# Kernel tuning notes

Measured on AMD Instinct MI355X. Metric: run time of the kernel, lower is better.

The kernel has to match this reference:

```python
import jax, jax.numpy as jnp
import numpy as np
from jax import lax

R = 25          # top-k hard attention cutoff
LBP_DAMP = 0.5  # damping factor for loopy BP
LBP_ITER = 5    # number of message-passing rounds
M, C, W, D = 400, 8, 100, 300  # mentions, candidates, ctxt window, vec size
H = 100         # nn_pem_interm_size


def setup_inputs() -> dict:
    key = jax.random.key(0)
    ks = jax.random.split(key, 12)
    ctxt_words = jax.random.randint(ks[0], (M, W), 0, 300000)
    ctxt_words_vec = jax.random.normal(ks[1], (M, W, D), jnp.float32)
    cand_entities = jax.random.randint(ks[2], (M, C), 0, 300000)
    cand_entities_vec = jax.random.normal(ks[3], (M, C, D), jnp.float32)
    p_e_m = -jax.random.uniform(ks[4], (M, C), jnp.float32) * 5.0  # log p(e|m)
    # learned params (A/B/C init to ones in torch; perturb slightly for generality)
    A_linear = 1.0 + 0.02 * jax.random.normal(ks[5], (D,), jnp.float32)
    B_linear = 1.0 + 0.02 * jax.random.normal(ks[6], (D,), jnp.float32)
    C_linear = 1.0 + 0.02 * jax.random.normal(ks[7], (D,), jnp.float32)
    W1 = jax.random.normal(ks[8], (H, 2), jnp.float32) * 0.5
    b1 = jax.random.normal(ks[9], (H,), jnp.float32) * 0.1
    W2 = jax.random.normal(ks[10], (1, H), jnp.float32) * 0.1
    b2 = jax.random.normal(ks[11], (1,), jnp.float32) * 0.1
    return {
        "ctxt_words": ctxt_words, "ctxt_words_vec": ctxt_words_vec,
        "cand_entities": cand_entities, "cand_entities_vec": cand_entities_vec,
        "p_e_m": p_e_m,
        "A_linear": A_linear, "B_linear": B_linear, "C_linear": C_linear,
        "W1": W1, "b1": b1, "W2": W2, "b2": b2,
    }


def _entity_context(ctxt_words_vec, cand_entities_vec, A_linear, B_linear):
    # u_vec[m,c,w] = <A*e_mc, w_mw>
    pre_u = cand_entities_vec * A_linear                       # [M,C,D]
    u_vec = jnp.einsum('mcd,mwd->mcw', pre_u, ctxt_words_vec)  # [M,C,W]
    u = u_vec.max(axis=1)                                      # [M,W]
    top_k = lax.top_k(u, R)[0]                                 # [M,R] sorted desc
    sketch = top_k[:, R - 1][:, None]                          # R-th largest
    minus = u - sketch
    minus = jnp.where(minus > 0, minus, -50.0)  # Threshold(0, -50)
    minus = minus + sketch
    beta = jax.nn.softmax(minus, axis=1)                        # [M,W]
    ctxt_full = jnp.einsum('mwd,mw->md', ctxt_words_vec, beta)  # [M,D]
    scores = jnp.einsum('mcd,md->mc', cand_entities_vec, ctxt_full * B_linear)
    return scores, beta


def reference(ctxt_words, ctxt_words_vec, cand_entities, cand_entities_vec,
              p_e_m, A_linear, B_linear, C_linear, W1, b1, W2, b2):
    scores, beta = _entity_context(ctxt_words_vec, cand_entities_vec,
                                   A_linear, B_linear)          # [M,C]
    # pairwise entity-entity scores
    flat = cand_entities_vec.reshape(M * C, D)
    pairwise = ((flat * C_linear) @ flat.T).reshape(M, C, M, C)  # [M,C,M,C]
    # unary[a,b,m,c] = scores[m,c]
    up = pairwise + scores[None, None, :, :]                     # [M,C,M,C]

    msg = jnp.zeros((M, C, M), jnp.float32)
    # mask[j,:,j] = 0 (self-exclusion)
    mask = 1.0 - jnp.eye(M, dtype=jnp.float32)[:, None, :]       # [M,1,M]
    for _ in range(LBP_ITER):
        crf_old = (1.0 - LBP_DAMP) * jnp.exp(msg)                # [M,C,M]
        s = msg.sum(axis=2)                                      # [M,C]
        new = up + s[None, None, :, :]                           # [M,C,M,C]
        sel = new.max(axis=3)                                    # [M,C,M]
        sel = jax.nn.log_softmax(sel, axis=1)
        sel = sel * mask
        msg = jnp.log(jnp.exp(sel) * LBP_DAMP + crf_old)

    global_message = msg.sum(axis=2)                             # [M,C]
    fgs = jax.nn.log_softmax(scores + global_message, axis=-1)   # [M,C]
    x = jnp.stack([fgs.reshape(-1), p_e_m.reshape(-1)], axis=1)  # [M*C,2]
    x = jax.nn.relu(x @ W1.T + b1)                               # [M*C,H]
    x = x @ W2.T + b2                                            # [M*C,1]
    return x.reshape(M, C)
```

## Files before the change

kernel.cpp:

```cpp
#include <hip/hip_runtime.h>
#include <hip/hip_bf16.h>
#include <math.h>

#define Mm 400
#define Cc 8
#define Ww 100
#define Dd 300
#define Hh 100
#define Rr 25
#define MC 3200
#define KP 320
#define LBP_ITERS 5
#define CTX_STRIDE 688

typedef _Float16 f16x8 __attribute__((ext_vector_type(8)));
typedef _Float16 f16x4 __attribute__((ext_vector_type(4)));
typedef float f32x4 __attribute__((ext_vector_type(4)));

__device__ __forceinline__ void gload16(const void* g, void* l) {
  __builtin_amdgcn_global_load_lds(
      (const __attribute__((address_space(1))) void*)g,
      (__attribute__((address_space(3))) void*)l, 16, 0, 0);
}

__global__ __launch_bounds__(256) void k_convert(
    const float* __restrict__ X,
    const float* __restrict__ Cl,
    const float* __restrict__ A,
    _Float16* __restrict__ Ah,
    _Float16* __restrict__ Bh,
    _Float16* __restrict__ AhA)
{
  int idx = blockIdx.x * 256 + threadIdx.x;
  if (idx >= MC * KP) return;
  int j = idx / KP, k = idx - j * KP;
  float x = 0.f, cl = 0.f, a = 0.f;
  if (k < Dd) { x = X[(size_t)j * Dd + k]; cl = Cl[k]; a = A[k]; }
  Bh[idx]  = (_Float16)x;
  Ah[idx]  = (_Float16)(x * cl);
  AhA[idx] = (_Float16)(x * a);
}

__global__ __launch_bounds__(64) void k_u(
    const float* __restrict__ ctxt_vec,
    const _Float16* __restrict__ candA,
    float* __restrict__ u)
{
  const int bx = blockIdx.x, m = blockIdx.y;
  const int w0 = bx * 16;
  const int tid = threadIdx.x;
  const int fr = tid & 15, fq = tid >> 4;
  __shared__ __align__(16) _Float16 candH[16 * (CTX_STRIDE / 2)];
  __shared__ __align__(16) _Float16 ctxtH[16 * (CTX_STRIDE / 2)];

  const _Float16* ca = candA + (size_t)m * Cc * KP;
#pragma unroll
  for (int e = tid; e < 320; e += 64) {
    int r = e / 40, j = e - r * 40;
    f16x8 v = *(const f16x8*)(ca + r * KP + j * 8);
    *(f16x8*)((char*)candH + r * CTX_STRIDE + j * 16) = v;
  }
  const float* cw = ctxt_vec + (size_t)m * Ww * Dd;
  const int nr = (w0 + 16 <= Ww) ? 16 : (Ww - w0);
  for (int e = tid; e < nr * 75; e += 64) {
    int r = e / 75, j = e - r * 75;
    float4 v = *(const float4*)(cw + (size_t)(w0 + r) * Dd + j * 4);
    f16x4 h = { (_Float16)v.x, (_Float16)v.y, (_Float16)v.z, (_Float16)v.w };
    *(f16x4*)((char*)ctxtH + r * CTX_STRIDE + j * 8) = h;
  }
  for (int e = tid; e < nr * 5; e += 64) {
    int r = e / 5, q = e - r * 5;
    f16x4 z = {};
    *(f16x4*)((char*)ctxtH + r * CTX_STRIDE + 600 + q * 8) = z;
  }
  __syncthreads();

  f32x4 acc = {};
#pragma unroll
  for (int s = 0; s < 10; ++s) {
    int kb = s * 64 + fq * 16;
    f16x8 af = *(const f16x8*)((const char*)candH + fr * CTX_STRIDE + kb);
    f16x8 bf = *(const f16x8*)((const char*)ctxtH + fr * CTX_STRIDE + kb);
    acc = __builtin_amdgcn_mfma_f32_16x16x32_f16(af, bf, acc, 0, 0, 0);
  }
  float v0 = fmaxf(fmaxf(acc[0], acc[1]), fmaxf(acc[2], acc[3]));
  if (fq >= 2) v0 = -1e30f;
  v0 = fmaxf(v0, __shfl_xor(v0, 16));
  if (fq == 0 && (w0 + fr) < Ww) u[m * 128 + w0 + fr] = v0;
}

__global__ __launch_bounds__(512) void k_escore(
    const float* __restrict__ u,
    const float* __restrict__ ctxt_vec,
    const float* __restrict__ cand_vec,
    const float* __restrict__ B,
    float* __restrict__ scores)
{
  const int m = blockIdx.x;
  const int tid = threadIdx.x;
  __shared__ float u_s[Ww];
  __shared__ float beta_s[Ww];
  __shared__ int   idx_s[Ww];
  __shared__ int   cnt_s[2];
  __shared__ __align__(16) float cf_part[6 * 300];
  __shared__ __align__(16) float cfB[304];

  const float* cw  = ctxt_vec + (size_t)m * Ww * Dd;
  const float* cev = cand_vec + (size_t)m * Cc * Dd;

  if (tid < Ww) u_s[tid] = u[m * 128 + tid];
  __syncthreads();

  if (tid < 64) {
    float a0 = u_s[tid];
    float a1 = (tid + 64 < Ww) ? u_s[tid + 64] : -1e30f;
    float q0 = a0, q1 = a1, sketch = 0.f;
    for (int r = 0; r < Rr; ++r) {
      float v; int idx;
      if (q1 > q0) { v = q1; idx = tid + 64; } else { v = q0; idx = tid; }
#pragma unroll
      for (int off = 1; off < 64; off <<= 1) {
        float ov = __shfl_xor(v, off);
        int   oi = __shfl_xor(idx, off);
        if (ov > v || (ov == v && oi < idx)) { v = ov; idx = oi; }
      }
      sketch = v;
      if (idx == tid) q0 = -1e30f;
      else if (idx == tid + 64) q1 = -1e30f;
    }
    float m0 = (a0 > sketch) ? a0 : sketch - 50.0f;
    float m1 = (tid + 64 < Ww) ? ((a1 > sketch) ? a1 : sketch - 50.0f) : -1e30f;
    float mx = fmaxf(m0, m1);
#pragma unroll
    for (int off = 1; off < 64; off <<= 1) mx = fmaxf(mx, __shfl_xor(mx, off));
    float e0 = expf(m0 - mx);
    float e1 = (tid + 64 < Ww) ? expf(m1 - mx) : 0.f;
    float s = e0 + e1;
#pragma unroll
    for (int off = 1; off < 64; off <<= 1) s += __shfl_xor(s, off);
    float inv = 1.0f / s;
    beta_s[tid] = e0 * inv;
    if (tid + 64 < Ww) beta_s[tid + 64] = e1 * inv;
  }
  __syncthreads();

  bool sel = false;
  unsigned long long bmask = 0;
  if (tid < 128) {
    sel = (tid < Ww) && (beta_s[tid] > 1e-12f);
    bmask = __ballot(sel);
    if ((tid & 63) == 0) cnt_s[tid >> 6] = (int)__popcll(bmask);
  }
  __syncthreads();
  if (tid < 128 && sel) {
    int lane = tid & 63;
    int base = (tid >> 6) ? cnt_s[0] : 0;
    int pos = base + (int)__popcll(bmask & ((1ull << lane) - 1ull));
    idx_s[pos] = tid;
  }
  __syncthreads();
  const int g = cnt_s[0] + cnt_s[1];

  if (tid < 450) {
    int tg = tid / 75, d4 = tid - tg * 75;
    f32x4 cf = {};
    for (int i = tg; i < g; i += 6) {
      int w = idx_s[i];
      float4 x = *(const float4*)(cw + (size_t)w * Dd + d4 * 4);
      float bw = beta_s[w];
      cf[0] += bw * x.x; cf[1] += bw * x.y; cf[2] += bw * x.z; cf[3] += bw * x.w;
    }
    *(f32x4*)&cf_part[(tg * 75 + d4) * 4] = cf;
  }
  __syncthreads();

  if (tid < 75) {
    f32x4 s4 = *(const f32x4*)&cf_part[tid * 4];
#pragma unroll
    for (int tg = 1; tg < 6; ++tg) s4 += *(const f32x4*)&cf_part[(tg * 75 + tid) * 4];
    float4 b4 = *(const float4*)(B + tid * 4);
    s4[0] *= b4.x; s4[1] *= b4.y; s4[2] *= b4.z; s4[3] *= b4.w;
    *(f32x4*)&cfB[tid * 4] = s4;
  }
  __syncthreads();

  {
    int c = tid >> 6, lane = tid & 63;
    float p = 0.f;
    for (int d4 = lane; d4 < 75; d4 += 64) {
      float4 x = *(const float4*)(cev + (size_t)c * Dd + d4 * 4);
      f32x4 f = *(const f32x4*)&cfB[d4 * 4];
      p += x.x * f[0] + x.y * f[1] + x.z * f[2] + x.w * f[3];
    }
#pragma unroll
    for (int off = 32; off; off >>= 1) p += __shfl_down(p, off);
    if (lane == 0) scores[m * Cc + c] = p;
  }
}

__global__ __launch_bounds__(256) void k_pairwise_mfma(
    const _Float16* __restrict__ Ah,
    const _Float16* __restrict__ Bh,
    _Float16* __restrict__ P)
{
  __shared__ __align__(16) _Float16 Sh[2][128 * 32];
  const int tid = threadIdx.x;
  const int wave = tid >> 6, lane = tid & 63;
  const int wr = wave >> 1, wc = wave & 1;
  const int row0 = blockIdx.y * 128, col0 = blockIdx.x * 128;

  f32x4 acc[4][4] = {};
  const int fr = lane & 15, fq = lane >> 4;
  const int koff = fq * 8;

  for (int kt = 0; kt < KP / 32; ++kt) {
    const int k0 = kt * 32;
#pragma unroll
    for (int i = 0; i < 2; ++i) {
      int e = i * 256 + tid;
      int r = e >> 2;
      int kc = (e & 3) << 3;
      gload16(Ah + (size_t)(row0 + r) * KP + k0 + kc, (char*)Sh[0] + e * 16);
      gload16(Bh + (size_t)(col0 + r) * KP + k0 + kc, (char*)Sh[1] + e * 16);
    }
    __syncthreads();

    f16x8 af[4], bfr[4];
#pragma unroll
    for (int mi = 0; mi < 4; ++mi)
      af[mi] = *(const f16x8*)&Sh[0][(wr * 64 + mi * 16 + fr) * 32 + koff];
#pragma unroll
    for (int ni = 0; ni < 4; ++ni)
      bfr[ni] = *(const f16x8*)&Sh[1][(wc * 64 + ni * 16 + fr) * 32 + koff];
#pragma unroll
    for (int mi = 0; mi < 4; ++mi)
#pragma unroll
      for (int ni = 0; ni < 4; ++ni)
        acc[mi][ni] = __builtin_amdgcn_mfma_f32_16x16x32_f16(
            af[mi], bfr[ni], acc[mi][ni], 0, 0, 0);
    __syncthreads();
  }

  _Float16* wtile = (_Float16*)((char*)Sh + wave * 4096);
#pragma unroll
  for (int h = 0; h < 2; ++h) {
    __syncthreads();
#pragma unroll
    for (int mi2 = 0; mi2 < 2; ++mi2) {
      int mi = h * 2 + mi2;
#pragma unroll
      for (int ni = 0; ni < 4; ++ni)
#pragma unroll
        for (int r = 0; r < 4; ++r)
          wtile[(mi2 * 16 + fq * 4 + r) * 64 + ni * 16 + fr] =
              (_Float16)acc[mi][ni][r];
    }
    __syncthreads();
#pragma unroll
    for (int t = 0; t < 4; ++t) {
      int q = t * 64 + lane;
      int lr = q >> 3, lc8 = (q & 7) * 8;
      f16x8 v = *(const f16x8*)&wtile[lr * 64 + lc8];
      size_t gr = (size_t)(row0 + wr * 64 + h * 32 + lr);
      size_t gc = (size_t)(col0 + wc * 64 + lc8);
      *(f16x8*)(P + gr * MC + gc) = v;
    }
  }
}

__global__ __launch_bounds__(128) void k_lbp(
    const _Float16* __restrict__ P,
    const float* __restrict__ scores,
    const float* __restrict__ pIn,
    float* __restrict__ pOut,
    _Float16* __restrict__ emsg,
    int first)
{
  const int aa = blockIdx.x, q = blockIdx.y;
  const int tid = threadIdx.x;
  __shared__ float red_s[2][Cc];

  float psum[Cc];
#pragma unroll
  for (int b = 0; b < Cc; ++b) psum[b] = 0.f;

  const int m = q * 100 + tid;
  if (tid < 100) {
    const int j8 = m * Cc;
    f32x4 s0 = *(const f32x4*)&scores[j8];
    f32x4 s1 = *(const f32x4*)&scores[j8 + 4];
    if (!first) {
#pragma unroll
      for (int p4 = 0; p4 < 4; ++p4) {
        s0 += *(const f32x4*)&pIn[p4 * MC + j8];
        s1 += *(const f32x4*)&pIn[p4 * MC + j8 + 4];
      }
    }
    float t[Cc];
#pragma unroll
    for (int b = 0; b < Cc; ++b) {
      f16x8 ph = *(const f16x8*)(P + (size_t)(aa * Cc + b) * MC + m * 8);
      float tb = fmaxf(fmaxf((float)ph[0] + s0[0], (float)ph[1] + s0[1]),
                       fmaxf((float)ph[2] + s0[2], (float)ph[3] + s0[3]));
      t[b] = fmaxf(tb, fmaxf(fmaxf((float)ph[4] + s1[0], (float)ph[5] + s1[1]),
                             fmaxf((float)ph[6] + s1[2], (float)ph[7] + s1[3])));
    }
    float mxt = t[0];
#pragma unroll
    for (int b = 1; b < Cc; ++b) mxt = fmaxf(mxt, t[b]);
    float se = 0.f;
#pragma unroll
    for (int b = 0; b < Cc; ++b) { float eb = expf(t[b] - mxt); t[b] = eb; se += eb; }
    float inv_se = 1.0f / se;
    bool self = (m == aa);

    _Float16* ep = emsg + ((size_t)aa * Mm + m) * Cc;
    f16x8 eo;
    if (!first) eo = *(const f16x8*)ep;
    f16x8 en;
#pragma unroll
    for (int b = 0; b < Cc; ++b) {
      float sel_e = self ? 1.0f : t[b] * inv_se;
      float old_e = first ? 1.0f : (float)eo[b];
      float nv = 0.5f * sel_e + 0.5f * old_e;
      en[b] = (_Float16)nv;
      psum[b] += logf(nv);
    }
    *(f16x8*)ep = en;
  }

  const int wave = tid >> 6, lane = tid & 63;
#pragma unroll
  for (int b = 0; b < Cc; ++b)
#pragma unroll
    for (int off = 32; off; off >>= 1) psum[b] += __shfl_down(psum[b], off);
  if (lane == 0)
#pragma unroll
    for (int b = 0; b < Cc; ++b) red_s[wave][b] = psum[b];
  __syncthreads();
  if (tid < Cc)
    pOut[q * MC + aa * Cc + tid] = red_s[0][tid] + red_s[1][tid];
}

__global__ __launch_bounds__(64) void k_final2(
    const float* __restrict__ scores,
    const float* __restrict__ pF,
    const float* __restrict__ pem,
    const float* __restrict__ W1,
    const float* __restrict__ b1,
    const float* __restrict__ W2,
    const float* __restrict__ b2,
    float* __restrict__ out)
{
  int m = blockIdx.x * 64 + threadIdx.x;
  if (m >= Mm) return;
  float f[Cc], pm[Cc];
#pragma unroll
  for (int c = 0; c < Cc; ++c) {
    int j = m * Cc + c;
    f[c] = scores[j] + pF[j] + pF[MC + j] + pF[2 * MC + j] + pF[3 * MC + j];
    pm[c] = pem[j];
  }
  float mx = f[0];
#pragma unroll
  for (int c = 1; c < Cc; ++c) mx = fmaxf(mx, f[c]);
  float se = 0.f;
#pragma unroll
  for (int c = 0; c < Cc; ++c) se += expf(f[c] - mx);
  float lse = mx + logf(se);
  float fgs[Cc], accv[Cc];
  float bb2 = b2[0];
#pragma unroll
  for (int c = 0; c < Cc; ++c) { fgs[c] = f[c] - lse; accv[c] = bb2; }
  for (int h = 0; h < Hh; ++h) {
    float w0 = W1[2 * h], w1 = W1[2 * h + 1], bb = b1[h], w2 = W2[h];
#pragma unroll
    for (int c = 0; c < Cc; ++c)
      accv[c] += w2 * fmaxf(fgs[c] * w0 + pm[c] * w1 + bb, 0.f);
  }
#pragma unroll
  for (int c = 0; c < Cc; ++c) out[m * Cc + c] = accv[c];
}

extern "C" void kernel_launch(void* const* d_in, const int* in_sizes, int n_in,
                              void* d_out, int out_size, void* d_ws, size_t ws_size,
                              hipStream_t stream) {
  const float* ctxt_vec = (const float*)d_in[1];
  const float* cand_vec = (const float*)d_in[3];
  const float* pem      = (const float*)d_in[4];
  const float* A        = (const float*)d_in[5];
  const float* B        = (const float*)d_in[6];
  const float* Cl       = (const float*)d_in[7];
  const float* W1       = (const float*)d_in[8];
  const float* b1       = (const float*)d_in[9];
  const float* W2       = (const float*)d_in[10];
  const float* b2       = (const float*)d_in[11];
  float* out = (float*)d_out;

  char* ws = (char*)d_ws;
  _Float16* P     = (_Float16*)(ws);
  _Float16* Ah    = (_Float16*)(ws + 20480000);
  _Float16* Bh    = (_Float16*)(ws + 20480000 + 2048000);
  _Float16* AhA   = (_Float16*)(ws);
  _Float16* emsg  = (_Float16*)(ws + 20480000);
  float*   scores = (float*)(ws + 25600000);
  float*   pp     = (float*)(ws + 25612800);
  float*   u      = (float*)(ws + 25720000);

  k_convert<<<(MC * KP + 255) / 256, 256, 0, stream>>>(cand_vec, Cl, A, Ah, Bh, AhA);
  k_u<<<dim3(7, Mm), 64, 0, stream>>>(ctxt_vec, AhA, u);
  k_escore<<<Mm, 512, 0, stream>>>(u, ctxt_vec, cand_vec, B, scores);

  dim3 g(MC / 128, MC / 128);
  k_pairwise_mfma<<<g, 256, 0, stream>>>(Ah, Bh, P);

  float* pp0 = pp;
  float* pp1 = pp + 4 * MC;
  for (int it = 0; it < LBP_ITERS; ++it) {
    float* pout = (it & 1) ? pp1 : pp0;
    float* pin  = (it & 1) ? pp0 : pp1;
    k_lbp<<<dim3(Mm, 4), 128, 0, stream>>>(
        P, scores, pin, pout, emsg, it == 0 ? 1 : 0);
  }
  k_final2<<<(Mm + 63) / 64, 64, 0, stream>>>(
      scores, pp0, pem, W1, b1, W2, b2, out);
}
```

Baseline: 113.8 us.

## Compute u scores in fp32 directly and split LBP blocks into single-wave chunks

The context-attention score kernel now reads fp32 candidate and context vectors directly and computes dot products with FP32 FMAs and wave shuffles, dropping the fp16 MFMA path and the extra AhA conversion output. This removes one fp16 array write from the convert kernel and the fp16 staging, at the cost of reading fp32 context data with scalar math. The LBP kernel is split into 8 partitions of 50 mentions per single-wave block, which drops the shared-memory reduction and __syncthreads. In exchange, the final and next-iteration kernels must sum 8 partial buffers instead of 4.

```diff
diff --git a/kernel.cpp b/kernel.cpp
--- a/kernel.cpp
+++ b/kernel.cpp
@@ -11,7 +11,6 @@
 #define MC 3200
 #define KP 320
 #define LBP_ITERS 5
-#define CTX_STRIDE 688
 
 typedef _Float16 f16x8 __attribute__((ext_vector_type(8)));
 typedef _Float16 f16x4 __attribute__((ext_vector_type(4)));
@@ -26,67 +25,65 @@
 __global__ __launch_bounds__(256) void k_convert(
     const float* __restrict__ X,
     const float* __restrict__ Cl,
-    const float* __restrict__ A,
     _Float16* __restrict__ Ah,
-    _Float16* __restrict__ Bh,
-    _Float16* __restrict__ AhA)
+    _Float16* __restrict__ Bh)
 {
   int idx = blockIdx.x * 256 + threadIdx.x;
   if (idx >= MC * KP) return;
   int j = idx / KP, k = idx - j * KP;
-  float x = 0.f, cl = 0.f, a = 0.f;
-  if (k < Dd) { x = X[(size_t)j * Dd + k]; cl = Cl[k]; a = A[k]; }
-  Bh[idx]  = (_Float16)x;
-  Ah[idx]  = (_Float16)(x * cl);
-  AhA[idx] = (_Float16)(x * a);
-}
-
-__global__ __launch_bounds__(64) void k_u(
+  float x = 0.f, cl = 0.f;
+  if (k < Dd) { x = X[(size_t)j * Dd + k]; cl = Cl[k]; }
+  Bh[idx] = (_Float16)x;
+  Ah[idx] = (_Float16)(x * cl);
+}
+
+__global__ __launch_bounds__(256) void k_u(
     const float* __restrict__ ctxt_vec,
-    const _Float16* __restrict__ candA,
+    const float* __restrict__ cand_vec,
+    const float* __restrict__ A,
     float* __restrict__ u)
 {
-  const int bx = blockIdx.x, m = blockIdx.y;
-  const int w0 = bx * 16;
+  const int m = blockIdx.y;
+  const int wbase = blockIdx.x * 25;
   const int tid = threadIdx.x;
-  const int fr = tid & 15, fq = tid >> 4;
-  __shared__ __align__(16) _Float16 candH[16 * (CTX_STRIDE / 2)];
-  __shared__ __align__(16) _Float16 ctxtH[16 * (CTX_STRIDE / 2)];
-
-  const _Float16* ca = candA + (size_t)m * Cc * KP;
-#pragma unroll
-  for (int e = tid; e < 320; e += 64) {
-    int r = e / 40, j = e - r * 40;
-    f16x8 v = *(const f16x8*)(ca + r * KP + j * 8);
-    *(f16x8*)((char*)candH + r * CTX_STRIDE + j * 16) = v;
-  }
-  const float* cw = ctxt_vec + (size_t)m * Ww * Dd;
-  const int nr = (w0 + 16 <= Ww) ? 16 : (Ww - w0);
-  for (int e = tid; e < nr * 75; e += 64) {
-    int r = e / 75, j = e - r * 75;
-    float4 v = *(const float4*)(cw + (size_t)(w0 + r) * Dd + j * 4);
-    f16x4 h = { (_Float16)v.x, (_Float16)v.y, (_Float16)v.z, (_Float16)v.w };
-    *(f16x4*)((char*)ctxtH + r * CTX_STRIDE + j * 8) = h;
-  }
-  for (int e = tid; e < nr * 5; e += 64) {
-    int r = e / 5, q = e - r * 5;
-    f16x4 z = {};
-    *(f16x4*)((char*)ctxtH + r * CTX_STRIDE + 600 + q * 8) = z;
-  }
-  __syncthreads();
-
-  f32x4 acc = {};
-#pragma unroll
-  for (int s = 0; s < 10; ++s) {
-    int kb = s * 64 + fq * 16;
-    f16x8 af = *(const f16x8*)((const char*)candH + fr * CTX_STRIDE + kb);
-    f16x8 bf = *(const f16x8*)((const char*)ctxtH + fr * CTX_STRIDE + kb);
-    acc = __builtin_amdgcn_mfma_f32_16x16x32_f16(af, bf, acc, 0, 0, 0);
-  }
-  float v0 = fmaxf(fmaxf(acc[0], acc[1]), fmaxf(acc[2], acc[3]));
-  if (fq >= 2) v0 = -1e30f;
-  v0 = fmaxf(v0, __shfl_xor(v0, 16));
-  if (fq == 0 && (w0 + fr) < Ww) u[m * 128 + w0 + fr] = v0;
+  const int wave = tid >> 6, l = tid & 63;
+  __shared__ __align__(16) float candA[Cc * 300];
+
+  const float* cev = cand_vec + (size_t)m * Cc * Dd;
+  for (int e = tid; e < 600; e += 256) {
+    int c = e / 75, d4 = e - c * 75;
+    float4 v = *(const float4*)(cev + c * Dd + d4 * 4);
+    float4 a4 = *(const float4*)(A + d4 * 4);
+    *(float4*)&candA[c * 300 + d4 * 4] =
+        make_float4(v.x * a4.x, v.y * a4.y, v.z * a4.z, v.w * a4.w);
+  }
+  __syncthreads();
+
+  const int cg = l >> 3;
+  const int d0 = l & 7;
+  const float* ca = &candA[cg * 300];
+
+  for (int wi = wave; wi < 25; wi += 4) {
+    const int w = wbase + wi;
+    const float* row = ctxt_vec + ((size_t)m * Ww + w) * Dd;
+    float acc = 0.f;
+#pragma unroll
+    for (int k = 0; k < 10; ++k) {
+      int d4 = d0 + k * 8;
+      if (d4 < 75) {
+        float4 x = *(const float4*)(row + d4 * 4);
+        float4 e = *(const float4*)&ca[d4 * 4];
+        acc += x.x * e.x + x.y * e.y + x.z * e.z + x.w * e.w;
+      }
+    }
+    acc += __shfl_xor(acc, 1);
+    acc += __shfl_xor(acc, 2);
+    acc += __shfl_xor(acc, 4);
+    acc = fmaxf(acc, __shfl_xor(acc, 8));
+    acc = fmaxf(acc, __shfl_xor(acc, 16));
+    acc = fmaxf(acc, __shfl_xor(acc, 32));
+    if (l == 0) u[m * 128 + w] = acc;
+  }
 }
 
 __global__ __launch_bounds__(512) void k_escore(
@@ -268,7 +265,7 @@
   }
 }
 
-__global__ __launch_bounds__(128) void k_lbp(
+__global__ __launch_bounds__(64) void k_lbp(
     const _Float16* __restrict__ P,
     const float* __restrict__ scores,
     const float* __restrict__ pIn,
@@ -278,22 +275,21 @@
 {
   const int aa = blockIdx.x, q = blockIdx.y;
   const int tid = threadIdx.x;
-  __shared__ float red_s[2][Cc];
 
   float psum[Cc];
 #pragma unroll
   for (int b = 0; b < Cc; ++b) psum[b] = 0.f;
 
-  const int m = q * 100 + tid;
-  if (tid < 100) {
+  const int m = q * 50 + tid;
+  if (tid < 50) {
     const int j8 = m * Cc;
     f32x4 s0 = *(const f32x4*)&scores[j8];
     f32x4 s1 = *(const f32x4*)&scores[j8 + 4];
     if (!first) {
 #pragma unroll
-      for (int p4 = 0; p4 < 4; ++p4) {
-        s0 += *(const f32x4*)&pIn[p4 * MC + j8];
-        s1 += *(const f32x4*)&pIn[p4 * MC + j8 + 4];
+      for (int p8 = 0; p8 < 8; ++p8) {
+        s0 += *(const f32x4*)&pIn[p8 * MC + j8];
+        s1 += *(const f32x4*)&pIn[p8 * MC + j8 + 4];
       }
     }
     float t[Cc];
@@ -329,17 +325,16 @@
     *(f16x8*)ep = en;
   }
 
-  const int wave = tid >> 6, lane = tid & 63;
 #pragma unroll
   for (int b = 0; b < Cc; ++b)
 #pragma unroll
-    for (int off = 32; off; off >>= 1) psum[b] += __shfl_down(psum[b], off);
-  if (lane == 0)
-#pragma unroll
-    for (int b = 0; b < Cc; ++b) red_s[wave][b] = psum[b];
-  __syncthreads();
-  if (tid < Cc)
-    pOut[q * MC + aa * Cc + tid] = red_s[0][tid] + red_s[1][tid];
+    for (int off = 32; off; off >>= 1) psum[b] += __shfl_xor(psum[b], off);
+  if (tid == 0) {
+    f32x4 o0 = { psum[0], psum[1], psum[2], psum[3] };
+    f32x4 o1 = { psum[4], psum[5], psum[6], psum[7] };
+    *(f32x4*)&pOut[q * MC + aa * Cc]     = o0;
+    *(f32x4*)&pOut[q * MC + aa * Cc + 4] = o1;
+  }
 }
 
 __global__ __launch_bounds__(64) void k_final2(
@@ -358,7 +353,10 @@
 #pragma unroll
   for (int c = 0; c < Cc; ++c) {
     int j = m * Cc + c;
-    f[c] = scores[j] + pF[j] + pF[MC + j] + pF[2 * MC + j] + pF[3 * MC + j];
+    float s = scores[j];
+#pragma unroll
+    for (int p8 = 0; p8 < 8; ++p8) s += pF[p8 * MC + j];
+    f[c] = s;
     pm[c] = pem[j];
   }
   float mx = f[0];
@@ -401,25 +399,24 @@
   _Float16* P     = (_Float16*)(ws);
   _Float16* Ah    = (_Float16*)(ws + 20480000);
   _Float16* Bh    = (_Float16*)(ws + 20480000 + 2048000);
-  _Float16* AhA   = (_Float16*)(ws);
   _Float16* emsg  = (_Float16*)(ws + 20480000);
   float*   scores = (float*)(ws + 25600000);
   float*   pp     = (float*)(ws + 25612800);
-  float*   u      = (float*)(ws + 25720000);
-
-  k_convert<<<(MC * KP + 255) / 256, 256, 0, stream>>>(cand_vec, Cl, A, Ah, Bh, AhA);
-  k_u<<<dim3(7, Mm), 64, 0, stream>>>(ctxt_vec, AhA, u);
+  float*   u      = (float*)(ws + 26022400);
+
+  k_convert<<<(MC * KP + 255) / 256, 256, 0, stream>>>(cand_vec, Cl, Ah, Bh);
+  k_u<<<dim3(4, Mm), 256, 0, stream>>>(ctxt_vec, cand_vec, A, u);
   k_escore<<<Mm, 512, 0, stream>>>(u, ctxt_vec, cand_vec, B, scores);
 
   dim3 g(MC / 128, MC / 128);
   k_pairwise_mfma<<<g, 256, 0, stream>>>(Ah, Bh, P);
 
   float* pp0 = pp;
-  float* pp1 = pp + 4 * MC;
+  float* pp1 = pp + 8 * MC;
   for (int it = 0; it < LBP_ITERS; ++it) {
     float* pout = (it & 1) ? pp1 : pp0;
     float* pin  = (it & 1) ? pp0 : pp1;
-    k_lbp<<<dim3(Mm, 4), 128, 0, stream>>>(
+    k_lbp<<<dim3(Mm, 8), 64, 0, stream>>>(
         P, scores, pin, pout, emsg, it == 0 ? 1 : 0);
   }
   k_final2<<<(Mm + 63) / 64, 64, 0, stream>>>(
```

New measurement: 117.4 us. 3.2% more time.
